# Kernel tuning notes

Hardware: AMD Instinct MI355X
Metric: run time of the kernel (lower is better)

## Reference

```python
import jax, jax.numpy as jnp
import numpy as np

N = 8192
DIMS = 128
HID = 64
NEG = -9e15


def setup_inputs() -> dict:
    key = jax.random.key(0)
    k_adj, k_h, k_w1, k_w2 = jax.random.split(key, 4)
    graph_info = (jax.random.uniform(k_adj, (N, N)) < 0.01).astype(jnp.float32)
    h = jax.random.normal(k_h, (N, DIMS), dtype=jnp.float32)
    # xavier-normal-ish init for the 2-layer scoring MLP (dims -> 64 -> 1)
    W1 = jax.random.normal(k_w1, (DIMS, HID), dtype=jnp.float32) * np.sqrt(2.0 / (DIMS + HID))
    b1 = jnp.zeros((HID,), dtype=jnp.float32)
    W2 = jax.random.normal(k_w2, (HID, 1), dtype=jnp.float32) * np.sqrt(2.0 / (HID + 1))
    b2 = jnp.zeros((1,), dtype=jnp.float32)
    return {"graph_info": graph_info, "h": h, "W1": W1, "b1": b1, "W2": W2, "b2": b2}


def reference(graph_info, h, W1, b1, W2, b2):
    # per-node MLP score: e_j for every node j  -> [N, 1]
    e = jnp.dot(jnp.maximum(jnp.dot(h, W1) + b1, 0.0), W2) + b2
    # e.transpose().repeat(N,1): row i sees scores of all columns j -> broadcast [1, N]
    scores = e[:, 0][None, :]
    # mask non-edges with large negative, softmax over neighbors (dim=-1)
    att = jnp.where(graph_info > 0, scores, jnp.float32(NEG))
    att = jax.nn.softmax(att, axis=-1)
    out = jnp.dot(att, h)  # [N, dims] aggregation
    # sum_flag == 1: rescale each row by its degree (diagflat(num) @ h)
    num = jnp.sum(graph_info, axis=-1)  # [N]
    out = num[:, None] * out
    return out
```

## Files before the change

### kernel.cpp

```cpp
#include <hip/hip_runtime.h>
#include <math.h>

#define NN 8192
#define DIMS 128
#define HID 64
#define CAP 192
#define NWAVES 4
#define NPHASE 4
#define WTOT 2048

typedef float f4v __attribute__((ext_vector_type(4)));
typedef float f2v __attribute__((ext_vector_type(2)));
typedef unsigned short u16x8 __attribute__((ext_vector_type(8)));
typedef unsigned long long u64;

__global__ __launch_bounds__(256) void score_kernel(
    const float* __restrict__ h, const float* __restrict__ W1,
    const float* __restrict__ b1, const float* __restrict__ W2,
    const float* __restrict__ b2, float* __restrict__ ee) {
  __shared__ float sW1[DIMS * HID];
  for (int i = threadIdx.x * 4; i < DIMS * HID; i += 1024)
    *(float4*)&sW1[i] = *(const float4*)&W1[i];
  __syncthreads();
  int wv = threadIdx.x >> 6, lane = threadIdx.x & 63;
  int j0 = blockIdx.x * 16 + wv * 4;
  const f4v* h4 = (const f4v*)(h + (size_t)j0 * DIMS);
  float bb = b1[lane];
  float a0 = bb, a1 = bb, a2 = bb, a3 = bb;
#pragma unroll 8
  for (int d4 = 0; d4 < 32; ++d4) {
    f4v v0 = h4[d4], v1 = h4[d4 + 32], v2 = h4[d4 + 64], v3 = h4[d4 + 96];
    float w0 = sW1[(d4 * 4 + 0) * HID + lane];
    float w1 = sW1[(d4 * 4 + 1) * HID + lane];
    float w2c = sW1[(d4 * 4 + 2) * HID + lane];
    float w3 = sW1[(d4 * 4 + 3) * HID + lane];
    a0 = fmaf(v0.x, w0, a0); a0 = fmaf(v0.y, w1, a0); a0 = fmaf(v0.z, w2c, a0); a0 = fmaf(v0.w, w3, a0);
    a1 = fmaf(v1.x, w0, a1); a1 = fmaf(v1.y, w1, a1); a1 = fmaf(v1.z, w2c, a1); a1 = fmaf(v1.w, w3, a1);
    a2 = fmaf(v2.x, w0, a2); a2 = fmaf(v2.y, w1, a2); a2 = fmaf(v2.z, w2c, a2); a2 = fmaf(v2.w, w3, a2);
    a3 = fmaf(v3.x, w0, a3); a3 = fmaf(v3.y, w1, a3); a3 = fmaf(v3.z, w2c, a3); a3 = fmaf(v3.w, w3, a3);
  }
  float w2 = W2[lane];
  float r0 = fmaxf(a0, 0.f) * w2, r1 = fmaxf(a1, 0.f) * w2;
  float r2 = fmaxf(a2, 0.f) * w2, r3 = fmaxf(a3, 0.f) * w2;
#pragma unroll
  for (int off = 32; off > 0; off >>= 1) {
    r0 += __shfl_xor(r0, off, 64);
    r1 += __shfl_xor(r1, off, 64);
    r2 += __shfl_xor(r2, off, 64);
    r3 += __shfl_xor(r3, off, 64);
  }
  if (lane == 0) {
    float bo = b2[0];
    ee[j0]     = expf(r0 + bo);
    ee[j0 + 1] = expf(r1 + bo);
    ee[j0 + 2] = expf(r2 + bo);
    ee[j0 + 3] = expf(r3 + bo);
  }
}


#define NIBBLE(v)                                                              \
  ((u64)(((__float_as_uint((v).x) >> 29) & 1u) |                               \
         ((__float_as_uint((v).y) >> 28) & 2u) |                               \
         ((__float_as_uint((v).z) >> 27) & 4u) |                               \
         ((__float_as_uint((v).w) >> 26) & 8u)))

__device__ __forceinline__ void gather_batch8(
    const unsigned short* sidx, int q, int cnt,
    const float* __restrict__ ee, const float* __restrict__ hb,
    float& ax, float& ay, float& z) {
  if (q >= cnt) return;
  u16x8 jv = *(const u16x8*)(sidx + q);
  int j[8];
#pragma unroll
  for (int k = 0; k < 8; ++k) j[k] = (q + k < cnt) ? (int)jv[k] : 0;
  float wv[8];
#pragma unroll
  for (int k = 0; k < 8; ++k) wv[k] = ee[j[k]];
  f2v hv[8];
#pragma unroll
  for (int k = 0; k < 8; ++k) hv[k] = *(const f2v*)(hb + (size_t)j[k] * DIMS);
#pragma unroll
  for (int k = 0; k < 8; ++k) {
    float m = (q + k < cnt) ? wv[k] : 0.f;
    z += m;
    ax = fmaf(m, hv[k].x, ax);
    ay = fmaf(m, hv[k].y, ay);
  }
}

__global__ __launch_bounds__(256) void fused_kernel(
    const float* __restrict__ graph, const float* __restrict__ h,
    const float* __restrict__ ee, float* __restrict__ out) {
  __shared__ unsigned short s_idx[NWAVES][2][CAP];
  int w = threadIdx.x >> 6, lane = threadIdx.x & 63;
  int g = blockIdx.x * NWAVES + w;
  const float* hb = h + lane * 2;
  u64 lt = (1ull << lane) - 1ull;

  int pcnt = 0, pbuf = 0, prow = 0;
  float ax = 0.f, ay = 0.f, z = 0.f;

#pragma unroll 1
  for (int p = 0; p < NPHASE; ++p) {
    int row = g + p * WTOT;
    const f4v* g4 = (const f4v*)(graph + (size_t)row * NN) + lane;
    u64 a0 = 0, a1 = 0;
    f4v c0 = g4[0], c1 = g4[64], c2 = g4[128], c3 = g4[192];
#pragma unroll
    for (int t = 0; t < 8; ++t) {
      f4v n0, n1, n2, n3;
      if (t < 7) {
        const f4v* nb2 = g4 + (t * 4 + 4) * 64;
        n0 = nb2[0]; n1 = nb2[64]; n2 = nb2[128]; n3 = nb2[192];
      }
      {
        u64 q0 = NIBBLE(c0), q1 = NIBBLE(c1), q2 = NIBBLE(c2), q3 = NIBBLE(c3);
        int c = t * 4;
        if (c < 16)     a0 |= q0 << (4 * (c & 15));       else a1 |= q0 << (4 * (c & 15));
        if (c + 1 < 16) a0 |= q1 << (4 * ((c + 1) & 15)); else a1 |= q1 << (4 * ((c + 1) & 15));
        if (c + 2 < 16) a0 |= q2 << (4 * ((c + 2) & 15)); else a1 |= q2 << (4 * ((c + 2) & 15));
        if (c + 3 < 16) a0 |= q3 << (4 * ((c + 3) & 15)); else a1 |= q3 << (4 * ((c + 3) & 15));
      }
      if (p > 0) {
        gather_batch8(&s_idx[w][pbuf][0], t * 16 + 0, pcnt, ee, hb, ax, ay, z);
        gather_batch8(&s_idx[w][pbuf][0], t * 16 + 8, pcnt, ee, hb, ax, ay, z);
      }
      if (t < 7) { c0 = n0; c1 = n1; c2 = n2; c3 = n3; }
    }
    if (p > 0) {
#pragma unroll 1
      for (int q = 128; q < pcnt; q += 8)
        gather_batch8(&s_idx[w][pbuf][0], q, pcnt, ee, hb, ax, ay, z);
      float scale = pcnt > 0 ? (float)pcnt / z : 0.f;
      f2v o2; o2.x = ax * scale; o2.y = ay * scale;
      *(f2v*)(out + (size_t)prow * DIMS + lane * 2) = o2;
    }
    {
      int t0 = (int)__popcll(a0), t1 = (int)__popcll(a1);
      int tot = t0 + t1, incl = tot;
#pragma unroll
      for (int d = 1; d < 64; d <<= 1) {
        int vsh = __shfl_up(incl, d, 64);
        if (lane >= d) incl += vsh;
      }
      int base = incl - tot;
      int cnt = __shfl(incl, 63, 64);
      unsigned short* dst = &s_idx[w][p & 1][0];
      int pidx = base;
      u64 m = a0;
      while (m) {
        int bit = __ffsll(m) - 1;
        int col = ((bit >> 2) << 8) + lane * 4 + (bit & 3);
        if (pidx < CAP) dst[pidx] = (unsigned short)col;
        ++pidx; m &= m - 1;
      }
      m = a1;
      while (m) {
        int bit = __ffsll(m) - 1;
        int col = 4096 + ((bit >> 2) << 8) + lane * 4 + (bit & 3);
        if (pidx < CAP) dst[pidx] = (unsigned short)col;
        ++pidx; m &= m - 1;
      }
      pcnt = cnt < CAP ? cnt : CAP;
      pbuf = p & 1;
      prow = row;
      ax = 0.f; ay = 0.f; z = 0.f;
    }
  }
#pragma unroll 1
  for (int q = 0; q < pcnt; q += 8)
    gather_batch8(&s_idx[w][pbuf][0], q, pcnt, ee, hb, ax, ay, z);
  float scale = pcnt > 0 ? (float)pcnt / z : 0.f;
  f2v o2; o2.x = ax * scale; o2.y = ay * scale;
  *(f2v*)(out + (size_t)prow * DIMS + lane * 2) = o2;
}

extern "C" void kernel_launch(void* const* d_in, const int* in_sizes, int n_in,
                              void* d_out, int out_size, void* d_ws, size_t ws_size,
                              hipStream_t stream) {
  const float* graph = (const float*)d_in[0];
  const float* h     = (const float*)d_in[1];
  const float* W1    = (const float*)d_in[2];
  const float* b1    = (const float*)d_in[3];
  const float* W2    = (const float*)d_in[4];
  const float* b2    = (const float*)d_in[5];
  float* out = (float*)d_out;
  float* ee  = (float*)d_ws;

  score_kernel<<<NN / 16, 256, 0, stream>>>(h, W1, b1, W2, b2, ee);
  fused_kernel<<<WTOT / NWAVES, 256, 0, stream>>>(graph, h, ee, out);
}
```

Measured before the change: 78.98 us.

## Split rows into producer scan waves and consumer gather waves via shared flags

Replaces the per-wave software pipeline, where each wave scanned a row while gathering the previous one over four phases, with warp specialization. Each block handles four rows: two waves scan the adjacency and build index lists, and two waves wait on volatile shared flags and then do the gather and aggregation. The grid grows to NN/4 blocks. The aim is more parallelism and overlap of streaming and gathering across waves. In exchange, half the waves sit idle while scanning runs, spin-waiting costs cycles, and each scan no longer has gather work interleaved to hide its latency.

```diff
diff --git a/kernel.cpp b/kernel.cpp
--- a/kernel.cpp
+++ b/kernel.cpp
@@ -5,9 +5,6 @@
 #define DIMS 128
 #define HID 64
 #define CAP 192
-#define NWAVES 4
-#define NPHASE 4
-#define WTOT 2048
 
 typedef float f4v __attribute__((ext_vector_type(4)));
 typedef float f2v __attribute__((ext_vector_type(2)));
@@ -58,7 +55,6 @@
   }
 }
 
-
 #define NIBBLE(v)                                                              \
   ((u64)(((__float_as_uint((v).x) >> 29) & 1u) |                               \
          ((__float_as_uint((v).y) >> 28) & 2u) |                               \
@@ -89,54 +85,42 @@
   }
 }
 
-__global__ __launch_bounds__(256) void fused_kernel(
+__global__ __launch_bounds__(256) void pc_kernel(
     const float* __restrict__ graph, const float* __restrict__ h,
     const float* __restrict__ ee, float* __restrict__ out) {
-  __shared__ unsigned short s_idx[NWAVES][2][CAP];
+  __shared__ unsigned short s_idx[4][CAP];
+  volatile __shared__ int s_flag[4];
   int w = threadIdx.x >> 6, lane = threadIdx.x & 63;
-  int g = blockIdx.x * NWAVES + w;
-  const float* hb = h + lane * 2;
-  u64 lt = (1ull << lane) - 1ull;
+  int rbase = blockIdx.x * 4;
+  if (threadIdx.x < 4) s_flag[threadIdx.x] = 0;
+  __syncthreads();
 
-  int pcnt = 0, pbuf = 0, prow = 0;
-  float ax = 0.f, ay = 0.f, z = 0.f;
-
+  if (w < 2) {
+    u64 lt = (1ull << lane) - 1ull;
 #pragma unroll 1
-  for (int p = 0; p < NPHASE; ++p) {
-    int row = g + p * WTOT;
-    const f4v* g4 = (const f4v*)(graph + (size_t)row * NN) + lane;
-    u64 a0 = 0, a1 = 0;
-    f4v c0 = g4[0], c1 = g4[64], c2 = g4[128], c3 = g4[192];
+    for (int i = 0; i < 2; ++i) {
+      int s = w * 2 + i;
+      int row = rbase + s;
+      const f4v* g4 = (const f4v*)(graph + (size_t)row * NN) + lane;
+      u64 a0 = 0, a1 = 0;
+      f4v c0 = g4[0], c1 = g4[64], c2 = g4[128], c3 = g4[192];
 #pragma unroll
-    for (int t = 0; t < 8; ++t) {
-      f4v n0, n1, n2, n3;
-      if (t < 7) {
-        const f4v* nb2 = g4 + (t * 4 + 4) * 64;
-        n0 = nb2[0]; n1 = nb2[64]; n2 = nb2[128]; n3 = nb2[192];
+      for (int t = 0; t < 8; ++t) {
+        f4v n0, n1, n2, n3;
+        if (t < 7) {
+          const f4v* nb2 = g4 + (t * 4 + 4) * 64;
+          n0 = nb2[0]; n1 = nb2[64]; n2 = nb2[128]; n3 = nb2[192];
+        }
+        {
+          u64 q0 = NIBBLE(c0), q1 = NIBBLE(c1), q2 = NIBBLE(c2), q3 = NIBBLE(c3);
+          int c = t * 4;
+          if (c < 16)     a0 |= q0 << (4 * (c & 15));       else a1 |= q0 << (4 * (c & 15));
+          if (c + 1 < 16) a0 |= q1 << (4 * ((c + 1) & 15)); else a1 |= q1 << (4 * ((c + 1) & 15));
+          if (c + 2 < 16) a0 |= q2 << (4 * ((c + 2) & 15)); else a1 |= q2 << (4 * ((c + 2) & 15));
+          if (c + 3 < 16) a0 |= q3 << (4 * ((c + 3) & 15)); else a1 |= q3 << (4 * ((c + 3) & 15));
+        }
+        if (t < 7) { c0 = n0; c1 = n1; c2 = n2; c3 = n3; }
       }
-      {
-        u64 q0 = NIBBLE(c0), q1 = NIBBLE(c1), q2 = NIBBLE(c2), q3 = NIBBLE(c3);
-        int c = t * 4;
-        if (c < 16)     a0 |= q0 << (4 * (c & 15));       else a1 |= q0 << (4 * (c & 15));
-        if (c + 1 < 16) a0 |= q1 << (4 * ((c + 1) & 15)); else a1 |= q1 << (4 * ((c + 1) & 15));
-        if (c + 2 < 16) a0 |= q2 << (4 * ((c + 2) & 15)); else a1 |= q2 << (4 * ((c + 2) & 15));
-        if (c + 3 < 16) a0 |= q3 << (4 * ((c + 3) & 15)); else a1 |= q3 << (4 * ((c + 3) & 15));
-      }
-      if (p > 0) {
-        gather_batch8(&s_idx[w][pbuf][0], t * 16 + 0, pcnt, ee, hb, ax, ay, z);
-        gather_batch8(&s_idx[w][pbuf][0], t * 16 + 8, pcnt, ee, hb, ax, ay, z);
-      }
-      if (t < 7) { c0 = n0; c1 = n1; c2 = n2; c3 = n3; }
-    }
-    if (p > 0) {
-#pragma unroll 1
-      for (int q = 128; q < pcnt; q += 8)
-        gather_batch8(&s_idx[w][pbuf][0], q, pcnt, ee, hb, ax, ay, z);
-      float scale = pcnt > 0 ? (float)pcnt / z : 0.f;
-      f2v o2; o2.x = ax * scale; o2.y = ay * scale;
-      *(f2v*)(out + (size_t)prow * DIMS + lane * 2) = o2;
-    }
-    {
       int t0 = (int)__popcll(a0), t1 = (int)__popcll(a1);
       int tot = t0 + t1, incl = tot;
 #pragma unroll
@@ -146,7 +130,7 @@
       }
       int base = incl - tot;
       int cnt = __shfl(incl, 63, 64);
-      unsigned short* dst = &s_idx[w][p & 1][0];
+      unsigned short* dst = &s_idx[s][0];
       int pidx = base;
       u64 m = a0;
       while (m) {
@@ -162,18 +146,29 @@
         if (pidx < CAP) dst[pidx] = (unsigned short)col;
         ++pidx; m &= m - 1;
       }
-      pcnt = cnt < CAP ? cnt : CAP;
-      pbuf = p & 1;
-      prow = row;
-      ax = 0.f; ay = 0.f; z = 0.f;
+      cnt = cnt < CAP ? cnt : CAP;
+      __threadfence_block();
+      if (lane == 0) s_flag[s] = cnt + 1;
+    }
+  } else {
+    const float* hb = h + lane * 2;
+#pragma unroll 1
+    for (int i = 0; i < 2; ++i) {
+      int s = (w - 2) * 2 + i;
+      int row = rbase + s;
+      int f;
+      while ((f = s_flag[s]) == 0) __builtin_amdgcn_s_sleep(1);
+      __threadfence_block();
+      int cnt = f - 1;
+      float ax = 0.f, ay = 0.f, z = 0.f;
+#pragma unroll 1
+      for (int q = 0; q < cnt; q += 8)
+        gather_batch8(&s_idx[s][0], q, cnt, ee, hb, ax, ay, z);
+      float scale = cnt > 0 ? (float)cnt / z : 0.f;
+      f2v o2; o2.x = ax * scale; o2.y = ay * scale;
+      *(f2v*)(out + (size_t)row * DIMS + lane * 2) = o2;
     }
   }
-#pragma unroll 1
-  for (int q = 0; q < pcnt; q += 8)
-    gather_batch8(&s_idx[w][pbuf][0], q, pcnt, ee, hb, ax, ay, z);
-  float scale = pcnt > 0 ? (float)pcnt / z : 0.f;
-  f2v o2; o2.x = ax * scale; o2.y = ay * scale;
-  *(f2v*)(out + (size_t)prow * DIMS + lane * 2) = o2;
 }
 
 extern "C" void kernel_launch(void* const* d_in, const int* in_sizes, int n_in,
@@ -189,5 +184,5 @@
   float* ee  = (float*)d_ws;
 
   score_kernel<<<NN / 16, 256, 0, stream>>>(h, W1, b1, W2, b2, ee);
-  fused_kernel<<<WTOT / NWAVES, 256, 0, stream>>>(graph, h, ee, out);
+  pc_kernel<<<NN / 4, 256, 0, stream>>>(graph, h, ee, out);
 }
```

Result: no change. 79.02 us (+0.1%).
